# Optimization experiments

Measured on AMD Instinct MI355X. Metric: run time of the kernel, lower is better.

The kernel has to match this reference:

```python
import jax, jax.numpy as jnp
import numpy as np

B, H0, D = 8192, 64, 32
HIDDEN = [128, 128, 128]


def setup_inputs() -> dict:
    key = jax.random.key(0)
    ks = jax.random.split(key, 4)
    x = jax.random.normal(ks[0], (B, H0, D), dtype=jnp.float32)
    # he_normal: std = sqrt(2 / fan_in), fan_in ~= h_i * h0 for a [h_{i+1}, h_i, h0] kernel
    hs = [H0] + HIDDEN
    kernels = []
    for i in range(len(HIDDEN)):
        fan_in = hs[i] * hs[0]
        std = np.sqrt(2.0 / fan_in).astype(np.float32)
        kernels.append(jax.random.normal(ks[i + 1], (hs[i + 1], hs[i], hs[0]), dtype=jnp.float32) * std)
    return {
        'x': x,
        'k0': kernels[0], 'k1': kernels[1], 'k2': kernels[2],
        'b0': jnp.zeros((HIDDEN[0],), jnp.float32),
        'b1': jnp.zeros((HIDDEN[1],), jnp.float32),
        'b2': jnp.zeros((HIDDEN[2],), jnp.float32),
    }


def _cin(x, kernels, biases):
    # x: (b, h0, d). Layer i: feature_map[b,k,d] = relu( sum_{g,h} x_i[b,g,d] * x_0[b,h,d] * K[k,g,h] + bias[k] )
    x0 = x
    xi = x
    pooled = []
    for K, bias in zip(kernels, biases):
        fm = jnp.einsum('bgd,bhd,kgh->bkd', xi, x0, K) + bias[None, :, None]
        fm = jax.nn.relu(fm)
        xi = fm
        pooled.append(jnp.sum(fm, axis=-1))  # (b, hk)
    return jnp.concatenate(pooled, axis=-1)  # (b, sum(hidden))


def reference(x, k0, k1, k2, b0, b1, b2):
    return _cin(x, (k0, k1, k2), (b0, b1, b2))
```

## Files before the change

kernel.cpp:

```cpp
#include <hip/hip_runtime.h>

typedef unsigned short ushort_t;
typedef unsigned int u32;
typedef __attribute__((ext_vector_type(8))) short bf16x8;
typedef __attribute__((ext_vector_type(4))) float f32x4;
typedef __attribute__((ext_vector_type(4))) u32 u32x4;

__device__ __forceinline__ float b2f(ushort_t u) {
    return __builtin_bit_cast(float, (u32)u << 16);
}
__device__ __forceinline__ ushort_t f2b_rne(float f) {
    u32 u = __builtin_bit_cast(u32, f);
    u32 r = u + 0x7FFFu + ((u >> 16) & 1u);
    return (ushort_t)(r >> 16);
}
__device__ __forceinline__ u32 pack_trunc(float p0, float p1) {
    return __builtin_amdgcn_perm(__builtin_bit_cast(u32, p1),
                                 __builtin_bit_cast(u32, p0), 0x07060302u);
}
__device__ __forceinline__ void gl_lds16(const ushort_t* g, ushort_t* l) {
    __builtin_amdgcn_global_load_lds(
        (const __attribute__((address_space(1))) u32*)g,
        (__attribute__((address_space(3))) u32*)l, 16, 0, 0);
}

__global__ void cin_prep_x0bf(const float* __restrict__ x, ushort_t* __restrict__ x0bf) {
    __shared__ float xs[64 * 33];
    const int b = blockIdx.x, t = threadIdx.x;
    const float4* src = (const float4*)(x + (size_t)b * 2048);
#pragma unroll
    for (int i = 0; i < 2; ++i) {
        float4 f = src[t + 256 * i];
        int e = (t + 256 * i) * 4;
        int h = e >> 5, d = e & 31;
        xs[h * 33 + d]     = f.x;
        xs[h * 33 + d + 1] = f.y;
        xs[h * 33 + d + 2] = f.z;
        xs[h * 33 + d + 3] = f.w;
    }
    __syncthreads();
    const int d = t >> 3, j8 = t & 7;
    u32 w[4];
#pragma unroll
    for (int q = 0; q < 4; ++q) {
        int h0 = j8 * 8 + 2 * q;
        w[q] = (u32)f2b_rne(xs[h0 * 33 + d]) | ((u32)f2b_rne(xs[(h0 + 1) * 33 + d]) << 16);
    }
    uint4 o; o.x = w[0]; o.y = w[1]; o.z = w[2]; o.w = w[3];
    *(uint4*)(x0bf + ((size_t)b * 32 + d) * 64 + j8 * 8) = o;
}

__global__ void cin_prep_k2(const float* __restrict__ K, ushort_t* __restrict__ Kp, int G) {
    const int g = blockIdx.x, t = threadIdx.x;
    const int k = t >> 1, j0 = (t & 1) * 16;
    const float* s = K + ((size_t)k * G + g) * 64 + j0 * 2;
    u32* dst = (u32*)(Kp + (size_t)g * 8192 + k * 64);
    const int swc = k & 7;
#pragma unroll
    for (int c = 0; c < 4; ++c) {
        u32 w[4];
#pragma unroll
        for (int q = 0; q < 4; ++q) {
            int e = (c * 4 + q) * 2;
            w[q] = (u32)f2b_rne(s[e]) | ((u32)f2b_rne(s[e + 1]) << 16);
        }
        uint4 o; o.x = w[0]; o.y = w[1]; o.z = w[2]; o.w = w[3];
        *(uint4*)(dst + (((j0 >> 2) + c) ^ swc) * 4) = o;
    }
}

template <int G, bool STORE_FM>
__launch_bounds__(256, 2)
__global__ void cin_layer2(const ushort_t* __restrict__ x0bf,
                           const ushort_t* __restrict__ xi_src,
                           const ushort_t* __restrict__ Kp,
                           const float* __restrict__ bias,
                           ushort_t* __restrict__ fm_out,
                           float* __restrict__ out,
                           int layer_off) {
    constexpr int XI_STRIDE = G + 8;
    __shared__ ushort_t k_lds[2][8192];
    __shared__ ushort_t xi_lds[128 * XI_STRIDE];

    const int t = threadIdx.x;
    const int wg = blockIdx.x;
    const int lane = t & 63;
    const int wave = t >> 6;
    const int wm = wave >> 1, wn = wave & 1;
    const int col = lane & 15, g4 = lane >> 4;
    const int swz = (col & 7) << 3;

    {
        constexpr int CPR = G / 8;
        constexpr int TOT = 128 * CPR;
        const size_t n0 = (size_t)wg * 128;
#pragma unroll
        for (int i = 0; i < TOT / 256; ++i) {
            int c = t + 256 * i;
            int row = c / CPR, sub = c % CPR;
            u32x4 v = *(const u32x4*)(xi_src + (n0 + row) * G + sub * 8);
            *(u32x4*)(xi_lds + row * XI_STRIDE + sub * 8) = v;
        }
    }
    {
        const ushort_t* src = Kp + (size_t)t * 8;
        ushort_t* dst = k_lds[0] + t * 8;
#pragma unroll
        for (int i = 0; i < 4; ++i) gl_lds16(src + i * 2048, dst + i * 2048);
    }
    float xb[4][16];
#pragma unroll
    for (int nf = 0; nf < 4; ++nf) {
        const size_t n_g = (size_t)wg * 128 + wn * 64 + nf * 16 + col;
#pragma unroll
        for (int ks2 = 0; ks2 < 2; ++ks2) {
            u32x4 v = *(const u32x4*)(x0bf + n_g * 64 + ks2 * 32 + g4 * 8);
#pragma unroll
            for (int q = 0; q < 4; ++q) {
                xb[nf][ks2 * 8 + 2 * q]     = __builtin_bit_cast(float, v[q] << 16);
                xb[nf][ks2 * 8 + 2 * q + 1] = __builtin_bit_cast(float, v[q] & 0xFFFF0000u);
            }
        }
    }

    f32x4 acc[4][4];
#pragma unroll
    for (int a = 0; a < 4; ++a)
#pragma unroll
        for (int b = 0; b < 4; ++b) acc[a][b] = (f32x4){0.f, 0.f, 0.f, 0.f};

    __syncthreads();

    for (int g = 0; g < G; ++g) {
        const int cur = g & 1;
        if (g + 1 < G) {
            const ushort_t* src = Kp + (size_t)(g + 1) * 8192 + (size_t)t * 8;
            ushort_t* dst = k_lds[cur ^ 1] + t * 8;
#pragma unroll
            for (int i = 0; i < 4; ++i) gl_lds16(src + i * 2048, dst + i * 2048);
        }
        float xif[4];
#pragma unroll
        for (int nf = 0; nf < 4; ++nf)
            xif[nf] = b2f(xi_lds[(wn * 64 + nf * 16 + col) * XI_STRIDE + g]) * 1.0019569f;
        bf16x8 bw[4][2];
#pragma unroll
        for (int nf = 0; nf < 4; ++nf)
#pragma unroll
            for (int ks2 = 0; ks2 < 2; ++ks2) {
                u32x4 wv;
#pragma unroll
                for (int q = 0; q < 4; ++q) {
                    float p0 = xb[nf][ks2 * 8 + 2 * q] * xif[nf];
                    float p1 = xb[nf][ks2 * 8 + 2 * q + 1] * xif[nf];
                    wv[q] = pack_trunc(p0, p1);
                }
                bw[nf][ks2] = __builtin_bit_cast(bf16x8, wv);
            }
#pragma unroll
        for (int ks2 = 0; ks2 < 2; ++ks2) {
            bf16x8 af[4];
#pragma unroll
            for (int mf = 0; mf < 4; ++mf) {
                const int row = wm * 64 + mf * 16 + col;
                af[mf] = *(const bf16x8*)(k_lds[cur] + row * 64 + ((ks2 * 32 + g4 * 8) ^ swz));
            }
#pragma unroll
            for (int mf = 0; mf < 4; ++mf)
#pragma unroll
                for (int nf = 0; nf < 4; ++nf)
                    acc[mf][nf] = __builtin_amdgcn_mfma_f32_16x16x32_bf16(
                        af[mf], bw[nf][ks2], acc[mf][nf], 0, 0, 0);
        }
        __syncthreads();
    }

#pragma unroll
    for (int mf = 0; mf < 4; ++mf) {
        const int kk = wm * 64 + mf * 16 + g4 * 4;
        const float4 bs = *(const float4*)(bias + kk);
        float pool[2][4] = {{0.f, 0.f, 0.f, 0.f}, {0.f, 0.f, 0.f, 0.f}};
#pragma unroll
        for (int nf = 0; nf < 4; ++nf) {
            const size_t n_g = (size_t)wg * 128 + wn * 64 + nf * 16 + col;
            float v[4];
#pragma unroll
            for (int r = 0; r < 4; ++r) {
                float vv = acc[mf][nf][r] + ((r == 0) ? bs.x : (r == 1) ? bs.y : (r == 2) ? bs.z : bs.w);
                vv = fmaxf(vv, 0.f);
                v[r] = vv;
                pool[nf >> 1][r] += vv;
            }
            if (STORE_FM) {
                uint2 ww;
                ww.x = (u32)f2b_rne(v[0]) | ((u32)f2b_rne(v[1]) << 16);
                ww.y = (u32)f2b_rne(v[2]) | ((u32)f2b_rne(v[3]) << 16);
                *(uint2*)(fm_out + n_g * 128 + kk) = ww;
            }
        }
#pragma unroll
        for (int bi = 0; bi < 2; ++bi) {
#pragma unroll
            for (int r = 0; r < 4; ++r) {
                float s = pool[bi][r];
                s += __shfl_xor(s, 1, 16);
                s += __shfl_xor(s, 2, 16);
                s += __shfl_xor(s, 4, 16);
                s += __shfl_xor(s, 8, 16);
                pool[bi][r] = s;
            }
            if (col == 0) {
                const long b = (long)wg * 4 + wn * 2 + bi;
                float4 o;
                o.x = pool[bi][0]; o.y = pool[bi][1]; o.z = pool[bi][2]; o.w = pool[bi][3];
                *(float4*)(out + b * 384 + layer_off + kk) = o;
            }
        }
    }
}

extern "C" void kernel_launch(void* const* d_in, const int* in_sizes, int n_in,
                              void* d_out, int out_size, void* d_ws, size_t ws_size,
                              hipStream_t stream) {
    const float* x  = (const float*)d_in[0];
    const float* k0 = (const float*)d_in[1];
    const float* k1 = (const float*)d_in[2];
    const float* k2 = (const float*)d_in[3];
    const float* bb0 = (const float*)d_in[4];
    const float* bb1 = (const float*)d_in[5];
    const float* bb2 = (const float*)d_in[6];
    float* out = (float*)d_out;
    char* ws = (char*)d_ws;

    ushort_t* x0bf = (ushort_t*)(ws);
    ushort_t* Kp0  = (ushort_t*)(ws + 33554432);
    ushort_t* Kp1  = (ushort_t*)(ws + 34603008);
    ushort_t* Kp2  = (ushort_t*)(ws + 36700160);
    ushort_t* fm0  = (ushort_t*)(ws + 38797312);
    ushort_t* fm1  = (ushort_t*)(ws + 105906176);

    cin_prep_x0bf<<<8192, 256, 0, stream>>>(x, x0bf);
    cin_prep_k2<<<64, 256, 0, stream>>>(k0, Kp0, 64);
    cin_prep_k2<<<128, 256, 0, stream>>>(k1, Kp1, 128);
    cin_prep_k2<<<128, 256, 0, stream>>>(k2, Kp2, 128);

    cin_layer2<64, true><<<2048, 256, 0, stream>>>(x0bf, x0bf, Kp0, bb0, fm0, out, 0);
    cin_layer2<128, true><<<2048, 256, 0, stream>>>(x0bf, fm0, Kp1, bb1, fm1, out, 128);
    cin_layer2<128, false><<<2048, 256, 0, stream>>>(x0bf, fm1, Kp2, bb2, (ushort_t*)nullptr, out, 256);
}
```

Baseline: 1.205 ms.

## Stream xi per-g from transposed layout, raise occupancy, pack-mul bf16 convert

The CIN layer kernel no longer stages the whole xi tile in LDS. Feature maps and x0 are now stored transposed (g-major, n contiguous), and each g-slice of xi is streamed into a small triple-buffered LDS ring with async global-to-LDS loads two iterations ahead. This shrinks LDS use so launch bounds can go from 2 to 3 blocks per CU. The scale and bf16 conversion now use packed v_pk_mul_f32 and v_cvt_pk_bf16_f32 (round-to-nearest instead of truncation plus a fudge factor), and MFMA issue is wrapped in s_setprio. The risk is that the feature-map store becomes scattered 2-byte writes with stride NTOT, and an extra prep pass over x is added.

Result: slower. 3.317 ms (+175.4%).

```diff
diff --git a/kernel.cpp b/kernel.cpp
--- a/kernel.cpp
+++ b/kernel.cpp
@@ -4,7 +4,10 @@
 typedef unsigned int u32;
 typedef __attribute__((ext_vector_type(8))) short bf16x8;
 typedef __attribute__((ext_vector_type(4))) float f32x4;
+typedef __attribute__((ext_vector_type(2))) float f32x2;
 typedef __attribute__((ext_vector_type(4))) u32 u32x4;
+
+#define NTOT 262144
 
 __device__ __forceinline__ float b2f(ushort_t u) {
     return __builtin_bit_cast(float, (u32)u << 16);
@@ -14,9 +17,12 @@
     u32 r = u + 0x7FFFu + ((u >> 16) & 1u);
     return (ushort_t)(r >> 16);
 }
-__device__ __forceinline__ u32 pack_trunc(float p0, float p1) {
-    return __builtin_amdgcn_perm(__builtin_bit_cast(u32, p1),
-                                 __builtin_bit_cast(u32, p0), 0x07060302u);
+__device__ __forceinline__ u32 scale_pack(f32x2 xp, f32x2 s) {
+    f32x2 d;
+    asm("v_pk_mul_f32 %0, %1, %2" : "=v"(d) : "v"(xp), "v"(s));
+    u32 r;
+    asm("v_cvt_pk_bf16_f32 %0, %1, %2" : "=v"(r) : "v"(d[0]), "v"(d[1]));
+    return r;
 }
 __device__ __forceinline__ void gl_lds16(const ushort_t* g, ushort_t* l) {
     __builtin_amdgcn_global_load_lds(
@@ -50,6 +56,18 @@
     *(uint4*)(x0bf + ((size_t)b * 32 + d) * 64 + j8 * 8) = o;
 }
 
+__global__ void cin_prep_x0T(const float* __restrict__ x, ushort_t* __restrict__ x0T) {
+    const int b = blockIdx.x, t = threadIdx.x;
+    const int h = t >> 2, c = t & 3;
+    const float* s = x + (size_t)b * 2048 + h * 32 + c * 8;
+    u32 w[4];
+#pragma unroll
+    for (int q = 0; q < 4; ++q)
+        w[q] = (u32)f2b_rne(s[2 * q]) | ((u32)f2b_rne(s[2 * q + 1]) << 16);
+    uint4 o; o.x = w[0]; o.y = w[1]; o.z = w[2]; o.w = w[3];
+    *(uint4*)(x0T + (size_t)h * NTOT + (size_t)b * 32 + c * 8) = o;
+}
+
 __global__ void cin_prep_k2(const float* __restrict__ K, ushort_t* __restrict__ Kp, int G) {
     const int g = blockIdx.x, t = threadIdx.x;
     const int k = t >> 1, j0 = (t & 1) * 16;
@@ -70,17 +88,16 @@
 }
 
 template <int G, bool STORE_FM>
-__launch_bounds__(256, 2)
-__global__ void cin_layer2(const ushort_t* __restrict__ x0bf,
+__launch_bounds__(256, 3)
+__global__ void cin_layer3(const ushort_t* __restrict__ x0bf,
                            const ushort_t* __restrict__ xi_src,
                            const ushort_t* __restrict__ Kp,
                            const float* __restrict__ bias,
                            ushort_t* __restrict__ fm_out,
                            float* __restrict__ out,
                            int layer_off) {
-    constexpr int XI_STRIDE = G + 8;
     __shared__ ushort_t k_lds[2][8192];
-    __shared__ ushort_t xi_lds[128 * XI_STRIDE];
+    __shared__ ushort_t xi_lds[3 * 128];
 
     const int t = threadIdx.x;
     const int wg = blockIdx.x;
@@ -89,36 +106,31 @@
     const int wm = wave >> 1, wn = wave & 1;
     const int col = lane & 15, g4 = lane >> 4;
     const int swz = (col & 7) << 3;
-
-    {
-        constexpr int CPR = G / 8;
-        constexpr int TOT = 128 * CPR;
-        const size_t n0 = (size_t)wg * 128;
-#pragma unroll
-        for (int i = 0; i < TOT / 256; ++i) {
-            int c = t + 256 * i;
-            int row = c / CPR, sub = c % CPR;
-            u32x4 v = *(const u32x4*)(xi_src + (n0 + row) * G + sub * 8);
-            *(u32x4*)(xi_lds + row * XI_STRIDE + sub * 8) = v;
-        }
-    }
+    const size_t n0 = (size_t)wg * 128;
+
     {
         const ushort_t* src = Kp + (size_t)t * 8;
         ushort_t* dst = k_lds[0] + t * 8;
 #pragma unroll
         for (int i = 0; i < 4; ++i) gl_lds16(src + i * 2048, dst + i * 2048);
-    }
-    float xb[4][16];
+        if (t < 16) {
+            gl_lds16(xi_src + n0 + t * 8, xi_lds + t * 8);
+            gl_lds16(xi_src + NTOT + n0 + t * 8, xi_lds + 128 + t * 8);
+        }
+    }
+    f32x2 xb2[4][8];
 #pragma unroll
     for (int nf = 0; nf < 4; ++nf) {
-        const size_t n_g = (size_t)wg * 128 + wn * 64 + nf * 16 + col;
+        const size_t n_g = n0 + wn * 64 + nf * 16 + col;
 #pragma unroll
         for (int ks2 = 0; ks2 < 2; ++ks2) {
             u32x4 v = *(const u32x4*)(x0bf + n_g * 64 + ks2 * 32 + g4 * 8);
 #pragma unroll
             for (int q = 0; q < 4; ++q) {
-                xb[nf][ks2 * 8 + 2 * q]     = __builtin_bit_cast(float, v[q] << 16);
-                xb[nf][ks2 * 8 + 2 * q + 1] = __builtin_bit_cast(float, v[q] & 0xFFFF0000u);
+                f32x2 p;
+                p[0] = __builtin_bit_cast(float, v[q] << 16);
+                p[1] = __builtin_bit_cast(float, v[q] & 0xFFFF0000u);
+                xb2[nf][ks2 * 4 + q] = p;
             }
         }
     }
@@ -131,48 +143,67 @@
 
     __syncthreads();
 
-    for (int g = 0; g < G; ++g) {
-        const int cur = g & 1;
-        if (g + 1 < G) {
-            const ushort_t* src = Kp + (size_t)(g + 1) * 8192 + (size_t)t * 8;
-            ushort_t* dst = k_lds[cur ^ 1] + t * 8;
+    float xifA[4], xifB[4];
+#pragma unroll
+    for (int nf = 0; nf < 4; ++nf)
+        xifA[nf] = b2f(xi_lds[wn * 64 + nf * 16 + col]);
+
+    int bi_nxt = 1, bi_iss = 2;
+
+    auto ITER = [&](int gg, float (&cur)[4], float (&nxt)[4]) {
+        if (gg + 1 < G) {
+            const ushort_t* src = Kp + (size_t)(gg + 1) * 8192 + (size_t)t * 8;
+            ushort_t* dst = k_lds[(gg + 1) & 1] + t * 8;
 #pragma unroll
             for (int i = 0; i < 4; ++i) gl_lds16(src + i * 2048, dst + i * 2048);
         }
-        float xif[4];
-#pragma unroll
-        for (int nf = 0; nf < 4; ++nf)
-            xif[nf] = b2f(xi_lds[(wn * 64 + nf * 16 + col) * XI_STRIDE + g]) * 1.0019569f;
+        if (gg + 2 < G && t < 16)
+            gl_lds16(xi_src + (size_t)(gg + 2) * NTOT + n0 + t * 8,
+                     xi_lds + bi_iss * 128 + t * 8);
         bf16x8 bw[4][2];
 #pragma unroll
-        for (int nf = 0; nf < 4; ++nf)
+        for (int nf = 0; nf < 4; ++nf) {
+            f32x2 s; s[0] = cur[nf]; s[1] = cur[nf];
 #pragma unroll
             for (int ks2 = 0; ks2 < 2; ++ks2) {
                 u32x4 wv;
 #pragma unroll
-                for (int q = 0; q < 4; ++q) {
-                    float p0 = xb[nf][ks2 * 8 + 2 * q] * xif[nf];
-                    float p1 = xb[nf][ks2 * 8 + 2 * q + 1] * xif[nf];
-                    wv[q] = pack_trunc(p0, p1);
-                }
+                for (int q = 0; q < 4; ++q)
+                    wv[q] = scale_pack(xb2[nf][ks2 * 4 + q], s);
                 bw[nf][ks2] = __builtin_bit_cast(bf16x8, wv);
             }
+        }
+        const ushort_t* kbuf = k_lds[gg & 1];
 #pragma unroll
         for (int ks2 = 0; ks2 < 2; ++ks2) {
             bf16x8 af[4];
 #pragma unroll
             for (int mf = 0; mf < 4; ++mf) {
                 const int row = wm * 64 + mf * 16 + col;
-                af[mf] = *(const bf16x8*)(k_lds[cur] + row * 64 + ((ks2 * 32 + g4 * 8) ^ swz));
-            }
+                af[mf] = *(const bf16x8*)(kbuf + row * 64 + ((ks2 * 32 + g4 * 8) ^ swz));
+            }
+            __builtin_amdgcn_s_setprio(1);
 #pragma unroll
             for (int mf = 0; mf < 4; ++mf)
 #pragma unroll
                 for (int nf = 0; nf < 4; ++nf)
                     acc[mf][nf] = __builtin_amdgcn_mfma_f32_16x16x32_bf16(
                         af[mf], bw[nf][ks2], acc[mf][nf], 0, 0, 0);
+            __builtin_amdgcn_s_setprio(0);
+        }
+        if (gg + 1 < G) {
+#pragma unroll
+            for (int nf = 0; nf < 4; ++nf)
+                nxt[nf] = b2f(xi_lds[bi_nxt * 128 + wn * 64 + nf * 16 + col]);
         }
         __syncthreads();
+        bi_nxt = bi_iss;
+        bi_iss = (bi_iss == 2) ? 0 : bi_iss + 1;
+    };
+
+    for (int g = 0; g < G; g += 2) {
+        ITER(g, xifA, xifB);
+        ITER(g + 1, xifB, xifA);
     }
 
 #pragma unroll
@@ -182,20 +213,13 @@
         float pool[2][4] = {{0.f, 0.f, 0.f, 0.f}, {0.f, 0.f, 0.f, 0.f}};
 #pragma unroll
         for (int nf = 0; nf < 4; ++nf) {
-            const size_t n_g = (size_t)wg * 128 + wn * 64 + nf * 16 + col;
-            float v[4];
+            const size_t n_g = n0 + wn * 64 + nf * 16 + col;
 #pragma unroll
             for (int r = 0; r < 4; ++r) {
                 float vv = acc[mf][nf][r] + ((r == 0) ? bs.x : (r == 1) ? bs.y : (r == 2) ? bs.z : bs.w);
                 vv = fmaxf(vv, 0.f);
-                v[r] = vv;
+                if (STORE_FM) fm_out[(size_t)(kk + r) * NTOT + n_g] = f2b_rne(vv);
                 pool[nf >> 1][r] += vv;
-            }
-            if (STORE_FM) {
-                uint2 ww;
-                ww.x = (u32)f2b_rne(v[0]) | ((u32)f2b_rne(v[1]) << 16);
-                ww.y = (u32)f2b_rne(v[2]) | ((u32)f2b_rne(v[3]) << 16);
-                *(uint2*)(fm_out + n_g * 128 + kk) = ww;
             }
         }
 #pragma unroll
@@ -238,13 +262,15 @@
     ushort_t* Kp2  = (ushort_t*)(ws + 36700160);
     ushort_t* fm0  = (ushort_t*)(ws + 38797312);
     ushort_t* fm1  = (ushort_t*)(ws + 105906176);
+    ushort_t* x0T  = fm1;
 
     cin_prep_x0bf<<<8192, 256, 0, stream>>>(x, x0bf);
+    cin_prep_x0T<<<8192, 256, 0, stream>>>(x, x0T);
     cin_prep_k2<<<64, 256, 0, stream>>>(k0, Kp0, 64);
     cin_prep_k2<<<128, 256, 0, stream>>>(k1, Kp1, 128);
     cin_prep_k2<<<128, 256, 0, stream>>>(k2, Kp2, 128);
 
-    cin_layer2<64, true><<<2048, 256, 0, stream>>>(x0bf, x0bf, Kp0, bb0, fm0, out, 0);
-    cin_layer2<128, true><<<2048, 256, 0, stream>>>(x0bf, fm0, Kp1, bb1, fm1, out, 128);
-    cin_layer2<128, false><<<2048, 256, 0, stream>>>(x0bf, fm1, Kp2, bb2, (ushort_t*)nullptr, out, 256);
-}
+    cin_layer3<64, true><<<2048, 256, 0, stream>>>(x0bf, x0T, Kp0, bb0, fm0, out, 0);
+    cin_layer3<128, true><<<2048, 256, 0, stream>>>(x0bf, fm0, Kp1, bb1, fm1, out, 128);
+    cin_layer3<128, false><<<2048, 256, 0, stream>>>(x0bf, fm1, Kp2, bb2, (ushort_t*)nullptr, out, 256);
+}
```

## Triple-buffer K and stream xi per pair of g via async LDS loads

Applied to the files above, without the earlier changes.

Restructures the layer kernel main loop to process two g-steps per iteration with a three-slot K ring buffer and a streamed xi buffer loaded through global_load_lds, replacing the full up-front xi tile in LDS. It keeps x0 as packed bf16 in registers and unpacks per step, uses v_cvt_pk_bf16_f32 (round-to-nearest) instead of truncation, drops the 1.0019569 scale, adds s_setprio around MFMAs, and uses explicit vmcnt waits with raw barriers. LDS usage shrinks and launch bounds move to three blocks per CU to raise occupancy, at the cost of more complex slot bookkeeping and tighter register pressure.

Result: slower. 2.547 ms (+111.5%).

```diff
diff --git a/kernel.cpp b/kernel.cpp
--- a/kernel.cpp
+++ b/kernel.cpp
@@ -6,22 +6,27 @@
 typedef __attribute__((ext_vector_type(4))) float f32x4;
 typedef __attribute__((ext_vector_type(4))) u32 u32x4;
 
-__device__ __forceinline__ float b2f(ushort_t u) {
-    return __builtin_bit_cast(float, (u32)u << 16);
-}
+#define NTOT 262144
+
 __device__ __forceinline__ ushort_t f2b_rne(float f) {
     u32 u = __builtin_bit_cast(u32, f);
     u32 r = u + 0x7FFFu + ((u >> 16) & 1u);
     return (ushort_t)(r >> 16);
 }
-__device__ __forceinline__ u32 pack_trunc(float p0, float p1) {
-    return __builtin_amdgcn_perm(__builtin_bit_cast(u32, p1),
-                                 __builtin_bit_cast(u32, p0), 0x07060302u);
+__device__ __forceinline__ u32 cvtpk(float lo, float hi) {
+    u32 r;
+    asm("v_cvt_pk_bf16_f32 %0, %1, %2" : "=v"(r) : "v"(lo), "v"(hi));
+    return r;
 }
 __device__ __forceinline__ void gl_lds16(const ushort_t* g, ushort_t* l) {
     __builtin_amdgcn_global_load_lds(
         (const __attribute__((address_space(1))) u32*)g,
         (__attribute__((address_space(3))) u32*)l, 16, 0, 0);
+}
+__device__ __forceinline__ void gl_lds4(const ushort_t* g, ushort_t* l) {
+    __builtin_amdgcn_global_load_lds(
+        (const __attribute__((address_space(1))) u32*)g,
+        (__attribute__((address_space(3))) u32*)l, 4, 0, 0);
 }
 
 __global__ void cin_prep_x0bf(const float* __restrict__ x, ushort_t* __restrict__ x0bf) {
@@ -70,17 +75,17 @@
 }
 
 template <int G, bool STORE_FM>
-__launch_bounds__(256, 2)
-__global__ void cin_layer2(const ushort_t* __restrict__ x0bf,
+__launch_bounds__(256, 3)
+__global__ void cin_layer4(const ushort_t* __restrict__ x0bf,
                            const ushort_t* __restrict__ xi_src,
                            const ushort_t* __restrict__ Kp,
                            const float* __restrict__ bias,
                            ushort_t* __restrict__ fm_out,
                            float* __restrict__ out,
                            int layer_off) {
-    constexpr int XI_STRIDE = G + 8;
-    __shared__ ushort_t k_lds[2][8192];
-    __shared__ ushort_t xi_lds[128 * XI_STRIDE];
+    constexpr int P = G / 2;
+    __shared__ ushort_t k_lds_flat[3 * 8192];
+    __shared__ ushort_t xi_flat[3 * 256];
 
     const int t = threadIdx.x;
     const int wg = blockIdx.x;
@@ -89,90 +94,127 @@
     const int wm = wave >> 1, wn = wave & 1;
     const int col = lane & 15, g4 = lane >> 4;
     const int swz = (col & 7) << 3;
-
-    {
-        constexpr int CPR = G / 8;
-        constexpr int TOT = 128 * CPR;
-        const size_t n0 = (size_t)wg * 128;
-#pragma unroll
-        for (int i = 0; i < TOT / 256; ++i) {
-            int c = t + 256 * i;
-            int row = c / CPR, sub = c % CPR;
-            u32x4 v = *(const u32x4*)(xi_src + (n0 + row) * G + sub * 8);
-            *(u32x4*)(xi_lds + row * XI_STRIDE + sub * 8) = v;
-        }
-    }
-    {
-        const ushort_t* src = Kp + (size_t)t * 8;
-        ushort_t* dst = k_lds[0] + t * 8;
+    const size_t n0 = (size_t)wg * 128;
+
+    auto issueK = [&](int kg, int slot) {
+        const ushort_t* src = Kp + (size_t)kg * 8192 + (size_t)t * 8;
+        ushort_t* dst = k_lds_flat + slot * 8192 + t * 8;
 #pragma unroll
         for (int i = 0; i < 4; ++i) gl_lds16(src + i * 2048, dst + i * 2048);
-    }
-    float xb[4][16];
+    };
+    auto issueXi = [&](int pi, int slot) {
+        const size_t r0 = n0 + lane;
+        gl_lds4(xi_src + r0 * G + pi * 2, xi_flat + slot * 256 + lane * 2);
+        gl_lds4(xi_src + (r0 + 64) * G + pi * 2, xi_flat + slot * 256 + 128 + lane * 2);
+    };
+
+    u32x4 pk4[8];
 #pragma unroll
     for (int nf = 0; nf < 4; ++nf) {
-        const size_t n_g = (size_t)wg * 128 + wn * 64 + nf * 16 + col;
+        const size_t n_g = n0 + wn * 64 + nf * 16 + col;
+#pragma unroll
+        for (int ks2 = 0; ks2 < 2; ++ks2)
+            pk4[nf * 2 + ks2] = *(const u32x4*)(x0bf + n_g * 64 + ks2 * 32 + g4 * 8);
+    }
+#pragma unroll
+    for (int i = 0; i < 8; ++i) {
+#pragma unroll
+        for (int q = 0; q < 4; ++q) asm volatile("" :: "v"(pk4[i][q]));
+    }
+
+    issueK(0, 0);
+    issueXi(0, 0);
+    issueK(1, 1);
+    issueXi((P > 1) ? 1 : 0, 1);
+
+    f32x4 acc[4][4];
+#pragma unroll
+    for (int a = 0; a < 4; ++a)
+#pragma unroll
+        for (int b = 0; b < 4; ++b) acc[a][b] = (f32x4){0.f, 0.f, 0.f, 0.f};
+
+    asm volatile("s_waitcnt vmcnt(6)" ::: "memory");
+    __builtin_amdgcn_s_barrier();
+    __builtin_amdgcn_sched_barrier(0);
+
+    u32 xr_cur[4], xr_nxt[4];
+#pragma unroll
+    for (int nf = 0; nf < 4; ++nf)
+        xr_cur[nf] = *(const u32*)(xi_flat + wn * 128 + (nf * 16 + col) * 2);
+
+    auto COMPUTE = [&](int rslot, const float* xif) {
+        const ushort_t* kbuf = k_lds_flat + rslot * 8192;
 #pragma unroll
         for (int ks2 = 0; ks2 < 2; ++ks2) {
-            u32x4 v = *(const u32x4*)(x0bf + n_g * 64 + ks2 * 32 + g4 * 8);
-#pragma unroll
-            for (int q = 0; q < 4; ++q) {
-                xb[nf][ks2 * 8 + 2 * q]     = __builtin_bit_cast(float, v[q] << 16);
-                xb[nf][ks2 * 8 + 2 * q + 1] = __builtin_bit_cast(float, v[q] & 0xFFFF0000u);
-            }
-        }
-    }
-
-    f32x4 acc[4][4];
-#pragma unroll
-    for (int a = 0; a < 4; ++a)
-#pragma unroll
-        for (int b = 0; b < 4; ++b) acc[a][b] = (f32x4){0.f, 0.f, 0.f, 0.f};
-
-    __syncthreads();
-
-    for (int g = 0; g < G; ++g) {
-        const int cur = g & 1;
-        if (g + 1 < G) {
-            const ushort_t* src = Kp + (size_t)(g + 1) * 8192 + (size_t)t * 8;
-            ushort_t* dst = k_lds[cur ^ 1] + t * 8;
-#pragma unroll
-            for (int i = 0; i < 4; ++i) gl_lds16(src + i * 2048, dst + i * 2048);
-        }
-        float xif[4];
-#pragma unroll
-        for (int nf = 0; nf < 4; ++nf)
-            xif[nf] = b2f(xi_lds[(wn * 64 + nf * 16 + col) * XI_STRIDE + g]) * 1.0019569f;
-        bf16x8 bw[4][2];
-#pragma unroll
-        for (int nf = 0; nf < 4; ++nf)
-#pragma unroll
-            for (int ks2 = 0; ks2 < 2; ++ks2) {
-                u32x4 wv;
+            bf16x8 bw[4], af[4];
+#pragma unroll
+            for (int nf = 0; nf < 4; ++nf) {
+                u32x4 o;
 #pragma unroll
                 for (int q = 0; q < 4; ++q) {
-                    float p0 = xb[nf][ks2 * 8 + 2 * q] * xif[nf];
-                    float p1 = xb[nf][ks2 * 8 + 2 * q + 1] * xif[nf];
-                    wv[q] = pack_trunc(p0, p1);
+                    u32 wv = pk4[nf * 2 + ks2][q];
+                    float lo = __builtin_bit_cast(float, wv << 16);
+                    float hi = __builtin_bit_cast(float, wv & 0xFFFF0000u);
+                    o[q] = cvtpk(lo * xif[nf], hi * xif[nf]);
                 }
-                bw[nf][ks2] = __builtin_bit_cast(bf16x8, wv);
-            }
-#pragma unroll
-        for (int ks2 = 0; ks2 < 2; ++ks2) {
-            bf16x8 af[4];
-#pragma unroll
-            for (int mf = 0; mf < 4; ++mf) {
-                const int row = wm * 64 + mf * 16 + col;
-                af[mf] = *(const bf16x8*)(k_lds[cur] + row * 64 + ((ks2 * 32 + g4 * 8) ^ swz));
-            }
+                bw[nf] = __builtin_bit_cast(bf16x8, o);
+            }
+#pragma unroll
+            for (int mf = 0; mf < 4; ++mf)
+                af[mf] = *(const bf16x8*)(kbuf + (wm * 64 + mf * 16 + col) * 64 +
+                                          ((ks2 * 32 + g4 * 8) ^ swz));
+            __builtin_amdgcn_s_setprio(1);
 #pragma unroll
             for (int mf = 0; mf < 4; ++mf)
 #pragma unroll
                 for (int nf = 0; nf < 4; ++nf)
                     acc[mf][nf] = __builtin_amdgcn_mfma_f32_16x16x32_bf16(
-                        af[mf], bw[nf][ks2], acc[mf][nf], 0, 0, 0);
-        }
-        __syncthreads();
+                        af[mf], bw[nf], acc[mf][nf], 0, 0, 0);
+            __builtin_amdgcn_s_setprio(0);
+        }
+    };
+
+    int m0 = 0, xs = 0;
+#pragma unroll 1
+    for (int p = 0; p < P; ++p) {
+        const int g = 2 * p;
+        {
+            int kg = g + 2; if (kg > G - 1) kg = G - 1;
+            int pi = p + 2; if (pi > P - 1) pi = P - 1;
+            int wK = m0 + 2; if (wK >= 3) wK -= 3;
+            int wX = xs + 2; if (wX >= 3) wX -= 3;
+            issueK(kg, wK);
+            issueXi(pi, wX);
+            float xif[4];
+#pragma unroll
+            for (int nf = 0; nf < 4; ++nf)
+                xif[nf] = __builtin_bit_cast(float, xr_cur[nf] << 16);
+            COMPUTE(m0, xif);
+            asm volatile("s_waitcnt vmcnt(6)" ::: "memory");
+            __builtin_amdgcn_s_barrier();
+            __builtin_amdgcn_sched_barrier(0);
+        }
+        {
+            int kg = g + 3; if (kg > G - 1) kg = G - 1;
+            issueK(kg, m0);
+            float xif[4];
+#pragma unroll
+            for (int nf = 0; nf < 4; ++nf)
+                xif[nf] = __builtin_bit_cast(float, xr_cur[nf] & 0xFFFF0000u);
+            int r1 = m0 + 1; if (r1 >= 3) r1 -= 3;
+            COMPUTE(r1, xif);
+            int xn = xs + 1; if (xn >= 3) xn -= 3;
+#pragma unroll
+            for (int nf = 0; nf < 4; ++nf)
+                xr_nxt[nf] = *(const u32*)(xi_flat + xn * 256 + wn * 128 + (nf * 16 + col) * 2);
+            asm volatile("s_waitcnt vmcnt(4)" ::: "memory");
+            __builtin_amdgcn_s_barrier();
+            __builtin_amdgcn_sched_barrier(0);
+#pragma unroll
+            for (int nf = 0; nf < 4; ++nf) xr_cur[nf] = xr_nxt[nf];
+            m0 += 2; if (m0 >= 3) m0 -= 3;
+            xs += 1; if (xs >= 3) xs -= 3;
+        }
     }
 
 #pragma unroll
@@ -182,7 +224,7 @@
         float pool[2][4] = {{0.f, 0.f, 0.f, 0.f}, {0.f, 0.f, 0.f, 0.f}};
 #pragma unroll
         for (int nf = 0; nf < 4; ++nf) {
-            const size_t n_g = (size_t)wg * 128 + wn * 64 + nf * 16 + col;
+            const size_t n_g = n0 + wn * 64 + nf * 16 + col;
             float v[4];
 #pragma unroll
             for (int r = 0; r < 4; ++r) {
@@ -244,7 +286,7 @@
     cin_prep_k2<<<128, 256, 0, stream>>>(k1, Kp1, 128);
     cin_prep_k2<<<128, 256, 0, stream>>>(k2, Kp2, 128);
 
-    cin_layer2<64, true><<<2048, 256, 0, stream>>>(x0bf, x0bf, Kp0, bb0, fm0, out, 0);
-    cin_layer2<128, true><<<2048, 256, 0, stream>>>(x0bf, fm0, Kp1, bb1, fm1, out, 128);
-    cin_layer2<128, false><<<2048, 256, 0, stream>>>(x0bf, fm1, Kp2, bb2, (ushort_t*)nullptr, out, 256);
-}
+    cin_layer4<64, true><<<2048, 256, 0, stream>>>(x0bf, x0bf, Kp0, bb0, fm0, out, 0);
+    cin_layer4<128, true><<<2048, 256, 0, stream>>>(x0bf, fm0, Kp1, bb1, fm1, out, 128);
+    cin_layer4<128, false><<<2048, 256, 0, stream>>>(x0bf, fm1, Kp2, bb2, (ushort_t*)nullptr, out, 256);
+}
```
